# Kernel tuning notes

Measured on AMD Instinct MI355X. Metric: run time of the kernel, lower is better.

Reference implementation:

```python
import jax, jax.numpy as jnp
import numpy as np

S, B, F, D, DF, NH, FH = 1152, 2, 128, 1024, 2048, 8, 4
SEP = 1024
EPS = 1e-5

def ln(x, g, b):
    m = x.mean(-1, keepdims=True)
    v = ((x - m) ** 2).mean(-1, keepdims=True)
    return (x - m) * jax.lax.rsqrt(v + EPS) * g + b

def mha(q, k, v, wi, bi, wo, bo, nh):
    # torch MultiheadAttention, batch_first=False: inputs (L, N, E)
    E = q.shape[-1]
    hd = E // nh
    qh = (q @ wi[:E].T + bi[:E]).reshape(q.shape[0], -1, nh, hd)
    kh = (k @ wi[E:2 * E].T + bi[E:2 * E]).reshape(k.shape[0], -1, nh, hd)
    vh = (v @ wi[2 * E:].T + bi[2 * E:]).reshape(k.shape[0], -1, nh, hd)
    s = jnp.einsum('qnhd,knhd->nhqk', qh, kh) / jnp.sqrt(jnp.float32(hd))
    a = jax.nn.softmax(s, axis=-1)
    o = jnp.einsum('nhqk,knhd->qnhd', a, vh).reshape(q.shape[0], -1, E)
    return o @ wo.T + bo

def setup_inputs() -> dict:
    key = jax.random.key(0)
    it = iter(jax.random.split(key, 40))
    def p(shape, s=0.02):
        return jax.random.normal(next(it), shape, jnp.float32) * s
    z = lambda *sh: jnp.zeros(sh, jnp.float32)
    o = lambda *sh: jnp.ones(sh, jnp.float32)
    return dict(
        src=jax.random.normal(next(it), (S, B, F), jnp.float32),
        sep=SEP,
        sa_wi=p((3 * D, D)), sa_bi=z(3 * D), sa_wo=p((D, D)), sa_bo=z(D),
        fa_wi=p((3 * F, F)), fa_bi=z(3 * F), fa_wo=p((F, F)), fa_bo=z(F),
        pl1_w=p((F, 1)), pl1_b=z(F),
        pl2_w=p((DF, F)), pl2_b=z(DF),
        pl3_w=p((1, DF)), pl3_b=z(1),
        pl4_w=p((DF, F)), pl4_b=z(DF),
        pl5_w=p((D, DF)), pl5_b=z(D),
        pl6_w=p((DF, D)), pl6_b=z(DF),
        pl7_w=p((D, DF)), pl7_b=z(D),
        l1_w=p((DF, D)), l1_b=z(DF),
        l2_w=p((F, DF)), l2_b=z(F),
        pn1_g=o(F), pn1_b=z(F),
        pn2_g=o(D), pn2_b=z(D),
        n1_g=o(D), n1_b=z(D),
        n2_g=o(F), n2_b=z(F),
    )

def _forward(src, sa_wi, sa_bi, sa_wo, sa_bo, fa_wi, fa_bi, fa_wo, fa_bo,
             pl1_w, pl1_b, pl2_w, pl2_b, pl3_w, pl3_b, pl4_w, pl4_b,
             pl5_w, pl5_b, pl6_w, pl6_b, pl7_w, pl7_b, l1_w, l1_b, l2_w, l2_b,
             pn1_g, pn1_b, pn2_g, pn2_b, n1_g, n1_b, n2_g, n2_b, sep):
    Sn, Bn, Fn = src.shape
    relu = jax.nn.relu
    # feature-wise attention: 'b h w -> w (b h) 1'
    x = jnp.transpose(src, (2, 0, 1)).reshape(Fn, Sn * Bn, 1)
    x = x @ pl1_w.T + pl1_b                       # (F, S*B, emsize_f)
    x = mha(x, x, x, fa_wi, fa_bi, fa_wo, fa_bo, FH)
    x = relu(x @ pl2_w.T + pl2_b) @ pl3_w.T + pl3_b  # (F, S*B, 1)
    x = jnp.transpose(x.reshape(Fn, Sn, Bn), (1, 2, 0))  # 'w (b h) 1 -> b h w'
    src1 = ln(x + src, pn1_g, pn1_b)              # (S, B, F)
    src1_ = relu(src1 @ pl4_w.T + pl4_b) @ pl5_w.T + pl5_b  # (S, B, D)
    li = src1_[:sep]
    sl = mha(li, li, li, sa_wi, sa_bi, sa_wo, sa_bo, NH)
    sl = ln(sl + li, pn2_g, pn2_b)
    sl_ = relu(sl @ pl6_w.T + pl6_b) @ pl7_w.T + pl7_b
    sl_ = ln(sl_, pn2_g, pn2_b) + sl
    sr = mha(src1_[sep:], sl_, sl_, sa_wi, sa_bi, sa_wo, sa_bo, NH)
    src2 = jnp.concatenate([sl, sr], axis=0)      # (S, B, D)
    so = ln(src2 + src1_, n1_g, n1_b)
    ff = relu(so @ l1_w.T + l1_b) @ l2_w.T + l2_b  # (S, B, F)
    return ln(src1 + ff, n2_g, n2_b)

def reference(src, sa_wi, sa_bi, sa_wo, sa_bo, fa_wi, fa_bi, fa_wo, fa_bo,
              pl1_w, pl1_b, pl2_w, pl2_b, pl3_w, pl3_b, pl4_w, pl4_b,
              pl5_w, pl5_b, pl6_w, pl6_b, pl7_w, pl7_b, l1_w, l1_b, l2_w, l2_b,
              pn1_g, pn1_b, pn2_g, pn2_b, n1_g, n1_b, n2_g, n2_b, sep):
    return _forward(src, sa_wi, sa_bi, sa_wo, sa_bo, fa_wi, fa_bi, fa_wo, fa_bo,
                    pl1_w, pl1_b, pl2_w, pl2_b, pl3_w, pl3_b, pl4_w, pl4_b,
                    pl5_w, pl5_b, pl6_w, pl6_b, pl7_w, pl7_b, l1_w, l1_b,
                    l2_w, l2_b, pn1_g, pn1_b, pn2_g, pn2_b, n1_g, n1_b,
                    n2_g, n2_b, sep)
```

## Files before the change

### kernel.cpp

```cpp
#include <hip/hip_runtime.h>

using s16x8 = __attribute__((ext_vector_type(8))) short;
using f32x4 = __attribute__((ext_vector_type(4))) float;
typedef unsigned short ushort_t;

__device__ __forceinline__ unsigned short f2bf(float f) {
    union { float f; unsigned u; } v; v.f = f;
    unsigned u = v.u + 0x7FFFu + ((v.u >> 16) & 1u);
    return (unsigned short)(u >> 16);
}
__device__ __forceinline__ float bf2f(unsigned short h) {
    union { unsigned u; float f; } v; v.u = ((unsigned)h) << 16;
    return v.f;
}

__device__ __forceinline__ float block_reduce(float v, int op, float* lds) {
    const int lane = threadIdx.x & 63;
    const int w    = threadIdx.x >> 6;
    const int nw   = blockDim.x >> 6;
#pragma unroll
    for (int off = 32; off > 0; off >>= 1) {
        float o = __shfl_down(v, off, 64);
        v = op ? fmaxf(v, o) : (v + o);
    }
    __syncthreads();
    if (lane == 0) lds[w] = v;
    __syncthreads();
    float r = lds[0];
    for (int i = 1; i < nw; i++) r = op ? fmaxf(r, lds[i]) : (r + lds[i]);
    return r;
}

__device__ __forceinline__ void load_lds16(const void* g, void* l) {
    __builtin_amdgcn_global_load_lds(
        (const __attribute__((address_space(1))) unsigned int*)g,
        (__attribute__((address_space(3))) unsigned int*)l, 16, 0, 0);
}

struct CvtArgs { const float* src[8]; ushort_t* dst[8]; int end[8]; };

__global__ __launch_bounds__(256)
void cvt_all(CvtArgs a)
{
    int i = blockIdx.x * 256 + threadIdx.x;
    int j = 0;
    while (j < 8 && i >= a.end[j]) j++;
    if (j >= 8) return;
    int li = i - (j ? a.end[j - 1] : 0);
    float4 v = *(const float4*)&a.src[j][(size_t)li * 4];
    ushort_t u[4] = { f2bf(v.x), f2bf(v.y), f2bf(v.z), f2bf(v.w) };
    *(uint2*)&a.dst[j][(size_t)li * 4] = *(uint2*)u;
}

template<bool RELU>
__global__ __launch_bounds__(256, 2)
void gemm_bf16(const ushort_t* __restrict__ A, const ushort_t* __restrict__ B,
               const float* __restrict__ bias, ushort_t* __restrict__ C,
               int M, int N, int K, int lda, int ldb, int ldc,
               long sAz, long sBz, long sCz, long sA2, long sB2, long sC2,
               int zshift, float alpha)
{
    __shared__ ushort_t As[128 * 32];
    __shared__ ushort_t Bs[128 * 32];

    const int tid = threadIdx.x;
    const int z   = blockIdx.z;
    const int z1  = z & ((1 << zshift) - 1);
    const int z2  = z >> zshift;
    const int m0  = blockIdx.x * 128;
    const int n0  = blockIdx.y * 128;

    const ushort_t* Ab = A + (size_t)z1 * sAz + (size_t)z2 * sA2 + (size_t)m0 * lda;
    const ushort_t* Bb = B + (size_t)z1 * sBz + (size_t)z2 * sB2 + (size_t)n0 * ldb;

    const int wave = tid >> 6, lane = tid & 63;
    const int wm = (wave & 1) * 64, wn = (wave >> 1) * 64;
    const int mi = lane & 15, quad = lane >> 4;

    f32x4 acc[4][4];
#pragma unroll
    for (int i = 0; i < 4; i++)
#pragma unroll
        for (int j = 0; j < 4; j++) acc[i][j] = (f32x4)0.f;

    const int r_0 = tid >> 2,           g_0 = (tid & 3) ^ ((r_0 >> 1) & 3);
    const int r_1 = (tid + 256) >> 2,   g_1 = (tid & 3) ^ ((r_1 >> 1) & 3);

    for (int k0 = 0; k0 < K; k0 += 32) {
        load_lds16(Ab + (size_t)r_0 * lda + k0 + g_0 * 8, &As[tid * 8]);
        load_lds16(Ab + (size_t)r_1 * lda + k0 + g_1 * 8, &As[(tid + 256) * 8]);
        load_lds16(Bb + (size_t)r_0 * ldb + k0 + g_0 * 8, &Bs[tid * 8]);
        load_lds16(Bb + (size_t)r_1 * ldb + k0 + g_1 * 8, &Bs[(tid + 256) * 8]);
        __syncthreads();

        s16x8 af[4], bfr[4];
#pragma unroll
        for (int t = 0; t < 4; t++) {
            int r = wm + t * 16 + mi;
            af[t] = *(const s16x8*)&As[r * 32 + ((quad ^ ((r >> 1) & 3)) * 8)];
        }
#pragma unroll
        for (int t = 0; t < 4; t++) {
            int r = wn + t * 16 + mi;
            bfr[t] = *(const s16x8*)&Bs[r * 32 + ((quad ^ ((r >> 1) & 3)) * 8)];
        }
#pragma unroll
        for (int tm = 0; tm < 4; tm++)
#pragma unroll
            for (int tn = 0; tn < 4; tn++)
                acc[tm][tn] = __builtin_amdgcn_mfma_f32_16x16x32_bf16(af[tm], bfr[tn], acc[tm][tn], 0, 0, 0);
        __syncthreads();
    }

#pragma unroll
    for (int tn = 0; tn < 4; tn++) {
        int col = n0 + wn + tn * 16 + mi;
        float bv = bias ? bias[col] : 0.f;
#pragma unroll
        for (int tm = 0; tm < 4; tm++) {
#pragma unroll
            for (int r = 0; r < 4; r++) {
                int row = m0 + wm + tm * 16 + quad * 4 + r;
                float v = acc[tm][tn][r] * alpha + bv;
                if (RELU) v = fmaxf(v, 0.f);
                C[(size_t)z1 * sCz + (size_t)z2 * sC2 + (size_t)row * ldc + col] = f2bf(v);
            }
        }
    }
}

__global__ __launch_bounds__(256)
void transp128(const ushort_t* __restrict__ in, ushort_t* __restrict__ out,
               int ldin, long inz1, long inz2, long outz)
{
    __shared__ ushort_t T[64][136];
    const int z = blockIdx.z, z1 = z & 7, z2 = z >> 3;
    const int n0 = blockIdx.x * 64;
    const ushort_t* ip = in + (size_t)z1 * inz1 + (size_t)z2 * inz2;
    const int rr = threadIdx.x >> 2, cg = (threadIdx.x & 3) * 32;
#pragma unroll
    for (int c = 0; c < 4; c++) {
        s16x8 v = *(const s16x8*)(ip + (size_t)(n0 + rr) * ldin + cg + c * 8);
        *(s16x8*)&T[rr][cg + c * 8] = v;
    }
    __syncthreads();
    const int d = threadIdx.x >> 1, j0 = (threadIdx.x & 1) * 32;
    ushort_t* op = out + (size_t)z * outz + (size_t)d * 1024 + n0 + j0;
#pragma unroll
    for (int c = 0; c < 4; c++) {
        s16x8 v;
#pragma unroll
        for (int j = 0; j < 8; j++) v[j] = (short)T[j0 + c * 8 + j][d];
        *(s16x8*)(op + c * 8) = v;
    }
}

__global__ void precomp1(const float* __restrict__ fa_wi, const float* __restrict__ fa_bi,
                         const float* __restrict__ pl1_w, const float* __restrict__ pl1_b,
                         float* __restrict__ consts)
{
    int j = threadIdx.x;
    if (j < 384) {
        float u = 0.f, v = 0.f;
        for (int k = 0; k < 128; k++) {
            float w = fa_wi[j * 128 + k];
            u = fmaf(w, pl1_w[k], u);
            v = fmaf(w, pl1_b[k], v);
        }
        consts[j]       = u;
        consts[512 + j] = v + fa_bi[j];
    }
}

__global__ void precomp2(const float* __restrict__ fa_wo, const float* __restrict__ fa_bo,
                         float* __restrict__ consts)
{
    int tid = threadIdx.x;
    const float* u = consts;
    const float* v = consts + 512;
    if (tid < 16) {
        int h = tid >> 2, w = tid & 3;
        const float* ql = (w < 2) ? u : v;
        const float* kr = ((w & 1) == 0) ? u : v;
        float acc = 0.f;
        for (int d = 0; d < 32; d++) acc += ql[h * 32 + d] * kr[128 + h * 32 + d];
        consts[1024 + tid] = acc * 0.17677669529663687f;
    }
#pragma unroll
    for (int h = 0; h < 4; h++) {
        float acc = 0.f;
        for (int d = 0; d < 32; d++)
            acc = fmaf(fa_wo[tid * 128 + h * 32 + d], u[256 + h * 32 + d], acc);
        consts[1088 + h * 128 + tid] = acc;
    }
    float c0 = fa_bo[tid];
    for (int idx = 0; idx < 128; idx++)
        c0 = fmaf(fa_wo[tid * 128 + idx], v[256 + idx], c0);
    consts[1600 + tid] = c0;
}

__global__ void precomp3(const float* __restrict__ pl2_w, const float* __restrict__ pl2_b,
                         const float* __restrict__ consts, ushort_t* __restrict__ Gb)
{
    int m = blockIdx.x * 256 + threadIdx.x;
    const float* wv = consts + 1088;
    const float* c0 = consts + 1600;
    float a0 = 0.f, ah[4] = {0.f, 0.f, 0.f, 0.f};
    for (int j = 0; j < 128; j++) {
        float w = pl2_w[m * 128 + j];
        ah[0] = fmaf(w, wv[0 * 128 + j], ah[0]);
        ah[1] = fmaf(w, wv[1 * 128 + j], ah[1]);
        ah[2] = fmaf(w, wv[2 * 128 + j], ah[2]);
        ah[3] = fmaf(w, wv[3 * 128 + j], ah[3]);
        a0    = fmaf(w, c0[j], a0);
    }
    ushort_t row[8];
#pragma unroll
    for (int h = 0; h < 4; h++) row[h] = f2bf(ah[h]);
    row[4] = f2bf(a0 + pl2_b[m]);
    row[5] = row[6] = row[7] = 0;
    *(uint4*)&Gb[m * 8] = *(uint4*)row;
}

__global__ __launch_bounds__(256, 3)
void feat_mlp_ln(const float* __restrict__ src, const float* __restrict__ consts,
                 const ushort_t* __restrict__ Gb, const float* __restrict__ pl3_w,
                 const float* __restrict__ pl3_b, const float* __restrict__ pn1_g,
                 const float* __restrict__ pn1_b, ushort_t* __restrict__ src1)
{
    __shared__ ushort_t Gs[2048 * 8];
    __shared__ ushort_t Ts[128 * 8];
    __shared__ float    wlds[2048];
    __shared__ float    sv[128];
    __shared__ float    ypart[2][128];
    __shared__ float    red[4];

    const int n   = blockIdx.x;
    const int tid = threadIdx.x;
    const int f   = tid & 127;
    const int hp  = tid >> 7;
    const bool act = (tid < 128);

#pragma unroll
    for (int p = 0; p < 8; p++) {
        int ci = tid + p * 256;
        load_lds16(Gb + (size_t)ci * 8, &Gs[ci * 8]);
    }
    load_lds16(pl3_w + tid * 4,          &wlds[tid * 4]);
    load_lds16(pl3_w + (tid + 256) * 4,  &wlds[(tid + 256) * 4]);

    if (act) sv[f] = src[n * 128 + f];
    __syncthreads();

    const float si = sv[f];
    float S1 = block_reduce(act ? si : 0.f, 0, red);
    float S2 = block_reduce(act ? si * si : 0.f, 0, red);
    float S3 = block_reduce(act ? si * si * si : 0.f, 0, red);
    float S4 = block_reduce(act ? si * si * si * si : 0.f, 0, red);
    float amax = block_reduce(act ? fabsf(si) : 0.f, 1, red);

    float ph[2];
#pragma unroll
    for (int hh = 0; hh < 2; hh++) {
        const int h = hp * 2 + hh;
        ph[hh] = consts[1024 + h * 4 + 0] * si + consts[1024 + h * 4 + 2];
    }
    float pmax = block_reduce(fmaxf(fabsf(ph[0]), fabsf(ph[1])), 1, red);

    float tt[2];
    if (pmax * amax < 0.25f) {
#pragma unroll
        for (int hh = 0; hh < 2; hh++) {
            float p = ph[hh];
            float num = fmaf(p, fmaf(p, fmaf(p, S4 * (1.f / 6.f), 0.5f * S3), S2), S1);
            float den = fmaf(p, fmaf(p, fmaf(p, S3 * (1.f / 6.f), 0.5f * S2), S1), 128.f);
            tt[hh] = num / den;
        }
    } else {
        float smax = block_reduce(act ? si : -3.4e38f, 1, red);
        float smin = -block_reduce(act ? -si : -3.4e38f, 1, red);
#pragma unroll
        for (int hh = 0; hh < 2; hh++) {
            float p = ph[hh];
            float m = fmaxf(p * smax, p * smin);
            float l = 0.f, t = 0.f;
            for (int j = 0; j < 128; j++) {
                float e = __expf(fmaf(p, sv[j], -m));
                l += e; t = fmaf(e, sv[j], t);
            }
            tt[hh] = t / l;
        }
    }

    Ts[f * 8 + hp * 2 + 0] = f2bf(tt[0]);
    Ts[f * 8 + hp * 2 + 1] = f2bf(tt[1]);
    if (act) {
        Ts[f * 8 + 4] = 0x3F80;
        Ts[f * 8 + 5] = 0; Ts[f * 8 + 6] = 0; Ts[f * 8 + 7] = 0;
    }
    __syncthreads();

    const int wave = tid >> 6, lane = tid & 63;
    const int mhalf = wave >> 1, wm = (wave & 1) * 64;
    const int mi = lane & 15, quad = lane >> 4;

    s16x8 af[4];
#pragma unroll
    for (int t = 0; t < 4; t++) {
        s16x8 v = *(const s16x8*)&Ts[(wm + t * 16 + mi) * 8];
        af[t] = (quad == 0) ? v : (s16x8)0;
    }

    float partial[4][4];
#pragma unroll
    for (int i = 0; i < 4; i++)
#pragma unroll
        for (int j = 0; j < 4; j++) partial[i][j] = 0.f;

#pragma unroll 2
    for (int mt = 0; mt < 64; mt++) {
        const int m0 = mhalf * 1024 + mt * 16;
        s16x8 bfr = *(const s16x8*)&Gs[(m0 + mi) * 8];
        f32x4 acc[4];
#pragma unroll
        for (int tm = 0; tm < 4; tm++)
            acc[tm] = __builtin_amdgcn_mfma_f32_16x16x32_bf16(af[tm], bfr, (f32x4)0.f, 0, 0, 0);
        float w = wlds[m0 + mi];
#pragma unroll
        for (int tm = 0; tm < 4; tm++)
#pragma unroll
            for (int r = 0; r < 4; r++)
                partial[tm][r] = fmaf(fmaxf(acc[tm][r], 0.f), w, partial[tm][r]);
    }

#pragma unroll
    for (int tm = 0; tm < 4; tm++)
#pragma unroll
        for (int r = 0; r < 4; r++) {
            float v = partial[tm][r];
            v += __shfl_xor(v, 8);
            v += __shfl_xor(v, 4);
            v += __shfl_xor(v, 2);
            v += __shfl_xor(v, 1);
            if (mi == 0) ypart[mhalf][wm + tm * 16 + quad * 4 + r] = v;
        }
    __syncthreads();

    float yv = 0.f;
    if (act)
        yv = ypart[0][f] + ypart[1][f] + pl3_b[0] + sv[f];
    float s  = block_reduce(yv, 0, red);
    float ss = block_reduce(yv * yv, 0, red);
    float mean = s * (1.f / 128.f);
    float var  = ss * (1.f / 128.f) - mean * mean;
    float inv  = rsqrtf(var + 1e-5f);
    if (act)
        src1[n * 128 + f] = f2bf((yv - mean) * inv * pn1_g[f] + pn1_b[f]);
}

template<bool OUTF32>
__global__ void ln_bf16(const ushort_t* __restrict__ a, const ushort_t* __restrict__ b,
                        const ushort_t* __restrict__ post, const float* __restrict__ g,
                        const float* __restrict__ beta, void* __restrict__ out, int D)
{
    __shared__ float red[4];
    const size_t row = blockIdx.x;
    const int tid = threadIdx.x;
    const int nit = D / blockDim.x;
    const ushort_t* ap = a + row * D;
    const ushort_t* bp = b ? b + row * D : nullptr;
    float xr[4];
    float s = 0.f, ss = 0.f;
    for (int i = 0; i < nit; i++) {
        int idx = i * blockDim.x + tid;
        float x = bf2f(ap[idx]) + (bp ? bf2f(bp[idx]) : 0.f);
        xr[i] = x; s += x; ss = fmaf(x, x, ss);
    }
    s  = block_reduce(s, 0, red);
    ss = block_reduce(ss, 0, red);
    float mean = s / D, var = ss / D - mean * mean;
    float inv = rsqrtf(var + 1e-5f);
    const ushort_t* pp = post ? post + row * D : nullptr;
    for (int i = 0; i < nit; i++) {
        int idx = i * blockDim.x + tid;
        float v = (xr[i] - mean) * inv * g[idx] + beta[idx];
        if (pp) v += bf2f(pp[idx]);
        if (OUTF32) ((float*)out)[row * D + idx] = v;
        else        ((ushort_t*)out)[row * D + idx] = f2bf(v);
    }
}

__global__ void ln_cat(const ushort_t* __restrict__ a1, const ushort_t* __restrict__ a2,
                       int split, const ushort_t* __restrict__ b,
                       const float* __restrict__ g, const float* __restrict__ beta,
                       ushort_t* __restrict__ out, int D)
{
    __shared__ float red[4];
    const int row = blockIdx.x;
    const int tid = threadIdx.x;
    const int nit = D / blockDim.x;
    const ushort_t* ap = (row < split) ? a1 + (size_t)row * D : a2 + (size_t)(row - split) * D;
    const ushort_t* bp = b + (size_t)row * D;
    float xr[4];
    float s = 0.f, ss = 0.f;
    for (int i = 0; i < nit; i++) {
        int idx = i * blockDim.x + tid;
        float x = bf2f(ap[idx]) + bf2f(bp[idx]);
        xr[i] = x; s += x; ss = fmaf(x, x, ss);
    }
    s  = block_reduce(s, 0, red);
    ss = block_reduce(ss, 0, red);
    float mean = s / D, var = ss / D - mean * mean;
    float inv = rsqrtf(var + 1e-5f);
    for (int i = 0; i < nit; i++) {
        int idx = i * blockDim.x + tid;
        out[(size_t)row * D + idx] = f2bf((xr[i] - mean) * inv * g[idx] + beta[idx]);
    }
}

__global__ __launch_bounds__(256)
void softmax_bf16(ushort_t* __restrict__ S)
{
    __shared__ float red[4];
    const size_t row = blockIdx.x;
    ushort_t* p = S + row * 1024;
    const int tid = threadIdx.x;
    uint2 u = *(const uint2*)&p[tid * 4];
    ushort_t* us = (ushort_t*)&u;
    float xr[4];
    float mx = -3.4e38f;
#pragma unroll
    for (int i = 0; i < 4; i++) { xr[i] = bf2f(us[i]); mx = fmaxf(mx, xr[i]); }
    mx = block_reduce(mx, 1, red);
    float sum = 0.f;
#pragma unroll
    for (int i = 0; i < 4; i++) { xr[i] = __expf(xr[i] - mx); sum += xr[i]; }
    sum = block_reduce(sum, 0, red);
    float inv = 1.f / sum;
#pragma unroll
    for (int i = 0; i < 4; i++) us[i] = f2bf(xr[i] * inv);
    *(uint2*)&p[tid * 4] = u;
}

static inline void gemm_go(hipStream_t s, const ushort_t* A, const ushort_t* B,
                           const float* bias, ushort_t* C,
                           int M, int N, int K, int lda, int ldb, int ldc,
                           long sAz, long sBz, long sCz, int Z, float alpha,
                           bool relu,
                           long sA2 = 0, long sB2 = 0, long sC2 = 0, int zshift = 0)
{
    dim3 g(M / 128, N / 128, Z), b(256);
    if (relu) gemm_bf16<true ><<<g, b, 0, s>>>(A, B, bias, C, M, N, K, lda, ldb, ldc, sAz, sBz, sCz, sA2, sB2, sC2, zshift, alpha);
    else      gemm_bf16<false><<<g, b, 0, s>>>(A, B, bias, C, M, N, K, lda, ldb, ldc, sAz, sBz, sCz, sA2, sB2, sC2, zshift, alpha);
}

extern "C" void kernel_launch(void* const* d_in, const int* in_sizes, int n_in,
                              void* d_out, int out_size, void* d_ws, size_t ws_size,
                              hipStream_t stream)
{
    const float* src   = (const float*)d_in[0];
    const float* sa_wi = (const float*)d_in[2];
    const float* sa_bi = (const float*)d_in[3];
    const float* sa_wo = (const float*)d_in[4];
    const float* sa_bo = (const float*)d_in[5];
    const float* fa_wi = (const float*)d_in[6];
    const float* fa_bi = (const float*)d_in[7];
    const float* fa_wo = (const float*)d_in[8];
    const float* fa_bo = (const float*)d_in[9];
    const float* pl1_w = (const float*)d_in[10];
    const float* pl1_b = (const float*)d_in[11];
    const float* pl2_w = (const float*)d_in[12];
    const float* pl2_b = (const float*)d_in[13];
    const float* pl3_w = (const float*)d_in[14];
    const float* pl3_b = (const float*)d_in[15];
    const float* pl4_w = (const float*)d_in[16];
    const float* pl4_b = (const float*)d_in[17];
    const float* pl5_w = (const float*)d_in[18];
    const float* pl5_b = (const float*)d_in[19];
    const float* pl6_w = (const float*)d_in[20];
    const float* pl6_b = (const float*)d_in[21];
    const float* pl7_w = (const float*)d_in[22];
    const float* pl7_b = (const float*)d_in[23];
    const float* l1_w  = (const float*)d_in[24];
    const float* l1_b  = (const float*)d_in[25];
    const float* l2_w  = (const float*)d_in[26];
    const float* l2_b  = (const float*)d_in[27];
    const float* pn1_g = (const float*)d_in[28];
    const float* pn1_b = (const float*)d_in[29];
    const float* pn2_g = (const float*)d_in[30];
    const float* pn2_b = (const float*)d_in[31];
    const float* n1_g  = (const float*)d_in[32];
    const float* n1_b  = (const float*)d_in[33];
    const float* n2_g  = (const float*)d_in[34];
    const float* n2_b  = (const float*)d_in[35];

    float* ws  = (float*)d_ws;
    float* out = (float*)d_out;

    float* CONSTS = ws;
    ushort_t* wsb = (ushort_t*)(ws + 16384);
    ushort_t* SAWIb  = wsb + 0;
    ushort_t* SAWOb  = wsb + 3145728;
    ushort_t* PL4b   = wsb + 4194304;
    ushort_t* PL5b   = wsb + 4456448;
    ushort_t* PL6b   = wsb + 6553600;
    ushort_t* PL7b   = wsb + 8650752;
    ushort_t* L1b    = wsb + 10747904;
    ushort_t* L2b    = wsb + 12845056;
    ushort_t* Gbb    = wsb + 13107200;
    ushort_t* SRC1b  = wsb + 13172736;
    ushort_t* HBIGb  = wsb + 13467648;
    ushort_t* SRC1_b = wsb + 18186240;
    ushort_t* QKVb   = wsb + 20545536;
    ushort_t* SBUFb  = wsb + 27623424;
    ushort_t* OBUFb  = wsb + 44400640;
    ushort_t* SLb    = wsb + 46497792;
    ushort_t* SLPb   = wsb + 48594944;
    ushort_t* SOb    = wsb + 50692096;
    ushort_t* FFb    = wsb + 53051392;

    {
        CvtArgs a;
        const float* srcs[8] = { sa_wi, sa_wo, pl4_w, pl5_w, pl6_w, pl7_w, l1_w, l2_w };
        ushort_t*    dsts[8] = { SAWIb, SAWOb, PL4b, PL5b, PL6b, PL7b, L1b, L2b };
        int          ns[8]   = { 3145728, 1048576, 262144, 2097152, 2097152, 2097152, 2097152, 262144 };
        int cum = 0;
        for (int i = 0; i < 8; i++) { a.src[i] = srcs[i]; a.dst[i] = dsts[i]; cum += ns[i] / 4; a.end[i] = cum; }
        cvt_all<<<(cum + 255) / 256, 256, 0, stream>>>(a);
    }

    precomp1<<<1, 384, 0, stream>>>(fa_wi, fa_bi, pl1_w, pl1_b, CONSTS);
    precomp2<<<1, 128, 0, stream>>>(fa_wo, fa_bo, CONSTS);
    precomp3<<<8, 256, 0, stream>>>(pl2_w, pl2_b, CONSTS, Gbb);
    feat_mlp_ln<<<2304, 256, 0, stream>>>(src, CONSTS, Gbb, pl3_w, pl3_b, pn1_g, pn1_b, SRC1b);

    gemm_go(stream, SRC1b, PL4b, pl4_b, HBIGb, 2304, 2048, 128, 128, 128, 2048, 0, 0, 0, 1, 1.f, true);
    gemm_go(stream, HBIGb, PL5b, pl5_b, SRC1_b, 2304, 1024, 2048, 2048, 2048, 1024, 0, 0, 0, 1, 1.f, false);

    gemm_go(stream, SRC1_b, SAWIb, sa_bi, QKVb, 2304, 3072, 1024, 1024, 1024, 3072, 0, 0, 0, 1, 1.f, false);
    const float iscale = 0.08838834764831845f;
    ushort_t* VT1 = HBIGb;
    transp128<<<dim3(16, 1, 16), 256, 0, stream>>>(QKVb + 2048, VT1, 6144, 128, 3072, 131072);
    gemm_go(stream, QKVb, QKVb + 1024, nullptr, SBUFb,
            1024, 1024, 128, 6144, 6144, 1024, 128, 128, 1048576, 16, iscale, false,
            3072, 3072, 8388608, 3);
    softmax_bf16<<<16384, 256, 0, stream>>>(SBUFb);
    gemm_go(stream, SBUFb, VT1, nullptr, OBUFb,
            1024, 128, 1024, 1024, 1024, 2048, 1048576, 131072, 128, 16, 1.f, false,
            8388608, 1048576, 1024, 3);
    gemm_go(stream, OBUFb, SAWOb, sa_bo, HBIGb, 2048, 1024, 1024, 1024, 1024, 1024, 0, 0, 0, 1, 1.f, false);
    ln_bf16<false><<<2048, 256, 0, stream>>>(HBIGb, SRC1_b, nullptr, pn2_g, pn2_b, SLb, 1024);

    gemm_go(stream, SLb, PL6b, pl6_b, HBIGb, 2048, 2048, 1024, 1024, 1024, 2048, 0, 0, 0, 1, 1.f, true);
    gemm_go(stream, HBIGb, PL7b, pl7_b, OBUFb, 2048, 1024, 2048, 2048, 2048, 1024, 0, 0, 0, 1, 1.f, false);
    ln_bf16<false><<<2048, 256, 0, stream>>>(OBUFb, nullptr, SLb, pn2_g, pn2_b, SLPb, 1024);

    ushort_t* KV2 = SBUFb;
    ushort_t* S2  = SBUFb + 4456448;
    ushort_t* SR  = SBUFb + 6553600;
    gemm_go(stream, SLPb, SAWIb + 1024 * 1024, sa_bi + 1024, KV2, 2048, 2048, 1024, 1024, 1024, 2048, 0, 0, 0, 1, 1.f, false);
    ushort_t* VT2 = HBIGb;
    transp128<<<dim3(16, 1, 16), 256, 0, stream>>>(KV2 + 1024, VT2, 4096, 128, 2048, 131072);
    gemm_go(stream, QKVb + 2048 * 3072, KV2, nullptr, S2,
            128, 1024, 128, 6144, 4096, 1024, 128, 128, 131072, 16, iscale, false,
            3072, 2048, 1048576, 3);
    softmax_bf16<<<2048, 256, 0, stream>>>(S2);
    gemm_go(stream, S2, VT2, nullptr, OBUFb,
            128, 128, 1024, 1024, 1024, 2048, 131072, 131072, 128, 16, 1.f, false,
            1048576, 1048576, 1024, 3);
    gemm_go(stream, OBUFb, SAWOb, sa_bo, SR, 256, 1024, 1024, 1024, 1024, 1024, 0, 0, 0, 1, 1.f, false);

    ln_cat<<<2304, 256, 0, stream>>>(SLb, SR, 2048, SRC1_b, n1_g, n1_b, SOb, 1024);

    gemm_go(stream, SOb, L1b, l1_b, HBIGb, 2304, 2048, 1024, 1024, 1024, 2048, 0, 0, 0, 1, 1.f, true);
    gemm_go(stream, HBIGb, L2b, l2_b, FFb, 2304, 128, 2048, 2048, 2048, 128, 0, 0, 0, 1, 1.f, false);
    ln_bf16<true><<<2304, 128, 0, stream>>>(FFb, SRC1b, nullptr, n2_g, n2_b, out, 128);
}
```

Measured before the change: 639.3 us.

## Add split-K GEMM path for low-occupancy GEMMs and widen feature MLP block

Adds a split-K variant of the bf16 GEMM that writes fp32 partials, plus reduction kernels (sum_cvt, and ln_part, which fuses the final partial sum with residual add and LayerNorm). It applies split-K to the pl5 GEMM, the small cross-attention PV and output projections, and the N=128 l2 GEMM, which otherwise launch too few blocks to fill the GPU. feat_mlp_ln moves to 512 threads, one head per 128 threads, and reads pl3_w directly instead of staging it in LDS. In exchange it adds extra fp32 partial traffic and extra launches, and the final LN now reads fp32 partials instead of a bf16 FF buffer.

```diff
diff --git a/kernel.cpp b/kernel.cpp
--- a/kernel.cpp
+++ b/kernel.cpp
@@ -52,10 +52,11 @@
     *(uint2*)&a.dst[j][(size_t)li * 4] = *(uint2*)u;
 }
 
-template<bool RELU>
+template<bool RELU, bool SPLITK>
 __global__ __launch_bounds__(256, 2)
 void gemm_bf16(const ushort_t* __restrict__ A, const ushort_t* __restrict__ B,
                const float* __restrict__ bias, ushort_t* __restrict__ C,
+               float* __restrict__ Cp, long pstride, int ksplen, int zmod,
                int M, int N, int K, int lda, int ldb, int ldc,
                long sAz, long sBz, long sCz, long sA2, long sB2, long sC2,
                int zshift, float alpha)
@@ -64,7 +65,9 @@
     __shared__ ushort_t Bs[128 * 32];
 
     const int tid = threadIdx.x;
-    const int z   = blockIdx.z;
+    int zz = blockIdx.z;
+    int ks = 0, z = zz;
+    if (SPLITK) { ks = zz / zmod; z = zz - ks * zmod; }
     const int z1  = z & ((1 << zshift) - 1);
     const int z2  = z >> zshift;
     const int m0  = blockIdx.x * 128;
@@ -86,7 +89,10 @@
     const int r_0 = tid >> 2,           g_0 = (tid & 3) ^ ((r_0 >> 1) & 3);
     const int r_1 = (tid + 256) >> 2,   g_1 = (tid & 3) ^ ((r_1 >> 1) & 3);
 
-    for (int k0 = 0; k0 < K; k0 += 32) {
+    const int kbeg = SPLITK ? ks * ksplen : 0;
+    const int kend = SPLITK ? kbeg + ksplen : K;
+
+    for (int k0 = kbeg; k0 < kend; k0 += 32) {
         load_lds16(Ab + (size_t)r_0 * lda + k0 + g_0 * 8, &As[tid * 8]);
         load_lds16(Ab + (size_t)r_1 * lda + k0 + g_1 * 8, &As[(tid + 256) * 8]);
         load_lds16(Bb + (size_t)r_0 * ldb + k0 + g_0 * 8, &Bs[tid * 8]);
@@ -112,21 +118,75 @@
         __syncthreads();
     }
 
-#pragma unroll
-    for (int tn = 0; tn < 4; tn++) {
-        int col = n0 + wn + tn * 16 + mi;
-        float bv = bias ? bias[col] : 0.f;
-#pragma unroll
-        for (int tm = 0; tm < 4; tm++) {
-#pragma unroll
-            for (int r = 0; r < 4; r++) {
-                int row = m0 + wm + tm * 16 + quad * 4 + r;
-                float v = acc[tm][tn][r] * alpha + bv;
-                if (RELU) v = fmaxf(v, 0.f);
-                C[(size_t)z1 * sCz + (size_t)z2 * sC2 + (size_t)row * ldc + col] = f2bf(v);
+    if (SPLITK) {
+        float* Cf = Cp + (size_t)ks * pstride + (size_t)z1 * sCz + (size_t)z2 * sC2;
+#pragma unroll
+        for (int tn = 0; tn < 4; tn++) {
+            int col = n0 + wn + tn * 16 + mi;
+#pragma unroll
+            for (int tm = 0; tm < 4; tm++)
+#pragma unroll
+                for (int r = 0; r < 4; r++) {
+                    int row = m0 + wm + tm * 16 + quad * 4 + r;
+                    Cf[(size_t)row * ldc + col] = acc[tm][tn][r] * alpha;
+                }
+        }
+    } else {
+#pragma unroll
+        for (int tn = 0; tn < 4; tn++) {
+            int col = n0 + wn + tn * 16 + mi;
+            float bv = bias ? bias[col] : 0.f;
+#pragma unroll
+            for (int tm = 0; tm < 4; tm++) {
+#pragma unroll
+                for (int r = 0; r < 4; r++) {
+                    int row = m0 + wm + tm * 16 + quad * 4 + r;
+                    float v = acc[tm][tn][r] * alpha + bv;
+                    if (RELU) v = fmaxf(v, 0.f);
+                    C[(size_t)z1 * sCz + (size_t)z2 * sC2 + (size_t)row * ldc + col] = f2bf(v);
+                }
             }
         }
     }
+}
+
+__global__ __launch_bounds__(256)
+void sum_cvt(const float* __restrict__ parts, long pstride, int P,
+             const float* __restrict__ bias, int ldc,
+             ushort_t* __restrict__ out, int total4)
+{
+    int i = blockIdx.x * 256 + threadIdx.x;
+    if (i >= total4) return;
+    size_t idx = (size_t)i * 4;
+    float4 s = *(const float4*)&parts[idx];
+    for (int p = 1; p < P; p++) {
+        float4 v = *(const float4*)&parts[(size_t)p * pstride + idx];
+        s.x += v.x; s.y += v.y; s.z += v.z; s.w += v.w;
+    }
+    if (bias) {
+        int col = (int)(idx % (size_t)ldc);
+        s.x += bias[col]; s.y += bias[col + 1]; s.z += bias[col + 2]; s.w += bias[col + 3];
+    }
+    ushort_t u[4] = { f2bf(s.x), f2bf(s.y), f2bf(s.z), f2bf(s.w) };
+    *(uint2*)&out[idx] = *(uint2*)u;
+}
+
+__global__ __launch_bounds__(128)
+void ln_part(const float* __restrict__ parts, long pstride, int P,
+             const float* __restrict__ bias, const ushort_t* __restrict__ resid,
+             const float* __restrict__ g, const float* __restrict__ beta,
+             float* __restrict__ out)
+{
+    __shared__ float red[4];
+    const int r = blockIdx.x, c = threadIdx.x;
+    float x = bias[c] + bf2f(resid[r * 128 + c]);
+    for (int p = 0; p < P; p++) x += parts[(size_t)p * pstride + (size_t)r * 128 + c];
+    float s  = block_reduce(x, 0, red);
+    float ss = block_reduce(x * x, 0, red);
+    float mean = s * (1.f / 128.f);
+    float var  = ss * (1.f / 128.f) - mean * mean;
+    float inv  = rsqrtf(var + 1e-5f);
+    out[(size_t)r * 128 + c] = (x - mean) * inv * g[c] + beta[c];
 }
 
 __global__ __launch_bounds__(256)
@@ -222,7 +282,7 @@
     *(uint4*)&Gb[m * 8] = *(uint4*)row;
 }
 
-__global__ __launch_bounds__(256, 3)
+__global__ __launch_bounds__(512, 4)
 void feat_mlp_ln(const float* __restrict__ src, const float* __restrict__ consts,
                  const ushort_t* __restrict__ Gb, const float* __restrict__ pl3_w,
                  const float* __restrict__ pl3_b, const float* __restrict__ pn1_g,
@@ -230,25 +290,21 @@
 {
     __shared__ ushort_t Gs[2048 * 8];
     __shared__ ushort_t Ts[128 * 8];
-    __shared__ float    wlds[2048];
     __shared__ float    sv[128];
-    __shared__ float    ypart[2][128];
-    __shared__ float    red[4];
+    __shared__ float    ypart[4][128];
+    __shared__ float    red[8];
 
     const int n   = blockIdx.x;
     const int tid = threadIdx.x;
     const int f   = tid & 127;
-    const int hp  = tid >> 7;
+    const int h   = tid >> 7;
     const bool act = (tid < 128);
 
 #pragma unroll
-    for (int p = 0; p < 8; p++) {
-        int ci = tid + p * 256;
+    for (int p = 0; p < 4; p++) {
+        int ci = tid + p * 512;
         load_lds16(Gb + (size_t)ci * 8, &Gs[ci * 8]);
     }
-    load_lds16(pl3_w + tid * 4,          &wlds[tid * 4]);
-    load_lds16(pl3_w + (tid + 256) * 4,  &wlds[(tid + 256) * 4]);
-
     if (act) sv[f] = src[n * 128 + f];
     __syncthreads();
 
@@ -259,41 +315,27 @@
     float S4 = block_reduce(act ? si * si * si * si : 0.f, 0, red);
     float amax = block_reduce(act ? fabsf(si) : 0.f, 1, red);
 
-    float ph[2];
-#pragma unroll
-    for (int hh = 0; hh < 2; hh++) {
-        const int h = hp * 2 + hh;
-        ph[hh] = consts[1024 + h * 4 + 0] * si + consts[1024 + h * 4 + 2];
-    }
-    float pmax = block_reduce(fmaxf(fabsf(ph[0]), fabsf(ph[1])), 1, red);
-
-    float tt[2];
+    const float p_ = consts[1024 + h * 4 + 0] * si + consts[1024 + h * 4 + 2];
+    float pmax = block_reduce(fabsf(p_), 1, red);
+
+    float tt;
     if (pmax * amax < 0.25f) {
-#pragma unroll
-        for (int hh = 0; hh < 2; hh++) {
-            float p = ph[hh];
-            float num = fmaf(p, fmaf(p, fmaf(p, S4 * (1.f / 6.f), 0.5f * S3), S2), S1);
-            float den = fmaf(p, fmaf(p, fmaf(p, S3 * (1.f / 6.f), 0.5f * S2), S1), 128.f);
-            tt[hh] = num / den;
-        }
+        float num = fmaf(p_, fmaf(p_, fmaf(p_, S4 * (1.f / 6.f), 0.5f * S3), S2), S1);
+        float den = fmaf(p_, fmaf(p_, fmaf(p_, S3 * (1.f / 6.f), 0.5f * S2), S1), 128.f);
+        tt = num / den;
     } else {
         float smax = block_reduce(act ? si : -3.4e38f, 1, red);
         float smin = -block_reduce(act ? -si : -3.4e38f, 1, red);
-#pragma unroll
-        for (int hh = 0; hh < 2; hh++) {
-            float p = ph[hh];
-            float m = fmaxf(p * smax, p * smin);
-            float l = 0.f, t = 0.f;
-            for (int j = 0; j < 128; j++) {
-                float e = __expf(fmaf(p, sv[j], -m));
-                l += e; t = fmaf(e, sv[j], t);
-            }
-            tt[hh] = t / l;
+        float m = fmaxf(p_ * smax, p_ * smin);
+        float l = 0.f, t = 0.f;
+        for (int j = 0; j < 128; j++) {
+            float e = __expf(fmaf(p_, sv[j], -m));
+            l += e; t = fmaf(e, sv[j], t);
         }
-    }
-
-    Ts[f * 8 + hp * 2 + 0] = f2bf(tt[0]);
-    Ts[f * 8 + hp * 2 + 1] = f2bf(tt[1]);
+        tt = t / l;
+    }
+
+    Ts[f * 8 + h] = f2bf(tt);
     if (act) {
         Ts[f * 8 + 4] = 0x3F80;
         Ts[f * 8 + 5] = 0; Ts[f * 8 + 6] = 0; Ts[f * 8 + 7] = 0;
@@ -301,7 +343,8 @@
     __syncthreads();
 
     const int wave = tid >> 6, lane = tid & 63;
-    const int mhalf = wave >> 1, wm = (wave & 1) * 64;
+    const int wm = (wave & 1) * 64;
+    const int mq = wave >> 1;
     const int mi = lane & 15, quad = lane >> 4;
 
     s16x8 af[4];
@@ -317,15 +360,15 @@
 #pragma unroll
         for (int j = 0; j < 4; j++) partial[i][j] = 0.f;
 
-#pragma unroll 2
-    for (int mt = 0; mt < 64; mt++) {
-        const int m0 = mhalf * 1024 + mt * 16;
+#pragma unroll 4
+    for (int mt = 0; mt < 32; mt++) {
+        const int m0 = mq * 512 + mt * 16;
         s16x8 bfr = *(const s16x8*)&Gs[(m0 + mi) * 8];
+        float w = pl3_w[m0 + mi];
         f32x4 acc[4];
 #pragma unroll
         for (int tm = 0; tm < 4; tm++)
             acc[tm] = __builtin_amdgcn_mfma_f32_16x16x32_bf16(af[tm], bfr, (f32x4)0.f, 0, 0, 0);
-        float w = wlds[m0 + mi];
 #pragma unroll
         for (int tm = 0; tm < 4; tm++)
 #pragma unroll
@@ -342,13 +385,13 @@
             v += __shfl_xor(v, 4);
             v += __shfl_xor(v, 2);
             v += __shfl_xor(v, 1);
-            if (mi == 0) ypart[mhalf][wm + tm * 16 + quad * 4 + r] = v;
+            if (mi == 0) ypart[mq][wm + tm * 16 + quad * 4 + r] = v;
         }
     __syncthreads();
 
     float yv = 0.f;
     if (act)
-        yv = ypart[0][f] + ypart[1][f] + pl3_b[0] + sv[f];
+        yv = ypart[0][f] + ypart[1][f] + ypart[2][f] + ypart[3][f] + pl3_b[0] + sv[f];
     float s  = block_reduce(yv, 0, red);
     float ss = block_reduce(yv * yv, 0, red);
     float mean = s * (1.f / 128.f);
@@ -447,11 +490,20 @@
                            int M, int N, int K, int lda, int ldb, int ldc,
                            long sAz, long sBz, long sCz, int Z, float alpha,
                            bool relu,
-                           long sA2 = 0, long sB2 = 0, long sC2 = 0, int zshift = 0)
-{
-    dim3 g(M / 128, N / 128, Z), b(256);
-    if (relu) gemm_bf16<true ><<<g, b, 0, s>>>(A, B, bias, C, M, N, K, lda, ldb, ldc, sAz, sBz, sCz, sA2, sB2, sC2, zshift, alpha);
-    else      gemm_bf16<false><<<g, b, 0, s>>>(A, B, bias, C, M, N, K, lda, ldb, ldc, sAz, sBz, sCz, sA2, sB2, sC2, zshift, alpha);
+                           long sA2 = 0, long sB2 = 0, long sC2 = 0, int zshift = 0,
+                           int ksplit = 1, float* Cp = nullptr, long pstride = 0)
+{
+    dim3 g(M / 128, N / 128, Z * ksplit), b(256);
+    int ksplen = K / ksplit;
+    if (ksplit > 1)
+        gemm_bf16<false, true ><<<g, b, 0, s>>>(A, B, nullptr, nullptr, Cp, pstride, ksplen, Z,
+            M, N, K, lda, ldb, ldc, sAz, sBz, sCz, sA2, sB2, sC2, zshift, alpha);
+    else if (relu)
+        gemm_bf16<true,  false><<<g, b, 0, s>>>(A, B, bias, C, nullptr, 0, 0, Z,
+            M, N, K, lda, ldb, ldc, sAz, sBz, sCz, sA2, sB2, sC2, zshift, alpha);
+    else
+        gemm_bf16<false, false><<<g, b, 0, s>>>(A, B, bias, C, nullptr, 0, 0, Z,
+            M, N, K, lda, ldb, ldc, sAz, sBz, sCz, sA2, sB2, sC2, zshift, alpha);
 }
 
 extern "C" void kernel_launch(void* const* d_in, const int* in_sizes, int n_in,
@@ -517,7 +569,7 @@
     ushort_t* SLb    = wsb + 46497792;
     ushort_t* SLPb   = wsb + 48594944;
     ushort_t* SOb    = wsb + 50692096;
-    ushort_t* FFb    = wsb + 53051392;
+    float* PARTS = (float*)SBUFb;
 
     {
         CvtArgs a;
@@ -532,10 +584,12 @@
     precomp1<<<1, 384, 0, stream>>>(fa_wi, fa_bi, pl1_w, pl1_b, CONSTS);
     precomp2<<<1, 128, 0, stream>>>(fa_wo, fa_bo, CONSTS);
     precomp3<<<8, 256, 0, stream>>>(pl2_w, pl2_b, CONSTS, Gbb);
-    feat_mlp_ln<<<2304, 256, 0, stream>>>(src, CONSTS, Gbb, pl3_w, pl3_b, pn1_g, pn1_b, SRC1b);
+    feat_mlp_ln<<<2304, 512, 0, stream>>>(src, CONSTS, Gbb, pl3_w, pl3_b, pn1_g, pn1_b, SRC1b);
 
     gemm_go(stream, SRC1b, PL4b, pl4_b, HBIGb, 2304, 2048, 128, 128, 128, 2048, 0, 0, 0, 1, 1.f, true);
-    gemm_go(stream, HBIGb, PL5b, pl5_b, SRC1_b, 2304, 1024, 2048, 2048, 2048, 1024, 0, 0, 0, 1, 1.f, false);
+    gemm_go(stream, HBIGb, PL5b, nullptr, nullptr, 2304, 1024, 2048, 2048, 2048, 1024, 0, 0, 0, 1, 1.f, false,
+            0, 0, 0, 0, 2, PARTS, 2359296);
+    sum_cvt<<<2304, 256, 0, stream>>>(PARTS, 2359296, 2, pl5_b, 1024, SRC1_b, 589824);
 
     gemm_go(stream, SRC1_b, SAWIb, sa_bi, QKVb, 2304, 3072, 1024, 1024, 1024, 3072, 0, 0, 0, 1, 1.f, false);
     const float iscale = 0.08838834764831845f;
@@ -565,14 +619,18 @@
             128, 1024, 128, 6144, 4096, 1024, 128, 128, 131072, 16, iscale, false,
             3072, 2048, 1048576, 3);
     softmax_bf16<<<2048, 256, 0, stream>>>(S2);
-    gemm_go(stream, S2, VT2, nullptr, OBUFb,
+    gemm_go(stream, S2, VT2, nullptr, nullptr,
             128, 128, 1024, 1024, 1024, 2048, 131072, 131072, 128, 16, 1.f, false,
-            1048576, 1048576, 1024, 3);
-    gemm_go(stream, OBUFb, SAWOb, sa_bo, SR, 256, 1024, 1024, 1024, 1024, 1024, 0, 0, 0, 1, 1.f, false);
+            1048576, 1048576, 1024, 3, 8, PARTS, 262144);
+    sum_cvt<<<256, 256, 0, stream>>>(PARTS, 262144, 8, nullptr, 2048, OBUFb, 65536);
+    gemm_go(stream, OBUFb, SAWOb, nullptr, nullptr, 256, 1024, 1024, 1024, 1024, 1024, 0, 0, 0, 1, 1.f, false,
+            0, 0, 0, 0, 8, PARTS, 262144);
+    sum_cvt<<<256, 256, 0, stream>>>(PARTS, 262144, 8, sa_bo, 1024, SR, 65536);
 
     ln_cat<<<2304, 256, 0, stream>>>(SLb, SR, 2048, SRC1_b, n1_g, n1_b, SOb, 1024);
 
     gemm_go(stream, SOb, L1b, l1_b, HBIGb, 2304, 2048, 1024, 1024, 1024, 2048, 0, 0, 0, 1, 1.f, true);
-    gemm_go(stream, HBIGb, L2b, l2_b, FFb, 2304, 128, 2048, 2048, 2048, 128, 0, 0, 0, 1, 1.f, false);
-    ln_bf16<true><<<2304, 128, 0, stream>>>(FFb, SRC1b, nullptr, n2_g, n2_b, out, 128);
-}
+    gemm_go(stream, HBIGb, L2b, nullptr, nullptr, 2304, 128, 2048, 2048, 2048, 128, 0, 0, 0, 1, 1.f, false,
+            0, 0, 0, 0, 8, PARTS, 294912);
+    ln_part<<<2304, 128, 0, stream>>>(PARTS, 294912, 8, l2_b, SRC1b, n2_g, n2_b, out);
+}
```

Measured after the change: 591.0 us. 7.5% less time.
